# Kernel tuning notes

Measured on AMD Instinct MI355X. Metric: run time of the kernel, lower is better.

## Reference

```python
import jax, jax.numpy as jnp
import numpy as np

B, T, I, H = 32, 1024, 512, 512


def setup_inputs() -> dict:
    key = jax.random.key(0)
    ks = jax.random.split(key, 9)
    s = 0.05  # xavier-ish scale for 512-dim layers
    return {
        "x": jax.random.normal(ks[0], (B, T, I), jnp.float32),
        "W_in_0": jax.random.normal(ks[1], (I, H), jnp.float32) * s,
        "b_in_0": jnp.zeros((H,), jnp.float32),
        "W_h_0": jax.random.normal(ks[2], (H, 2 * H), jnp.float32) * s,
        "b_h_0": jnp.zeros((2 * H,), jnp.float32),
        "W_in_1": jax.random.normal(ks[3], (H, H), jnp.float32) * s,
        "b_in_1": jnp.zeros((H,), jnp.float32),
        "W_h_1": jax.random.normal(ks[4], (H, 2 * H), jnp.float32) * s,
        "b_h_1": jnp.zeros((2 * H,), jnp.float32),
    }


def _cell(ti, m_prev, c_prev, W_h, b_h, hid):
    # ti: transformed input [B,H]; gates from previous m (the "hidden")
    gates = m_prev @ W_h + b_h                 # [B,2H]
    retain = jax.nn.sigmoid(gates[:, :hid])
    merge = jax.nn.sigmoid(gates[:, hid:])
    c_next = jnp.tanh(c_prev + retain * ti)
    m_next = (1.0 - merge) * ti + merge * c_next
    return m_next, c_next


def reference(x, W_in_0, b_in_0, W_h_0, b_h_0, W_in_1, b_in_1, W_h_1, b_h_1):
    b, t, _ = x.shape
    hid = W_in_0.shape[1]
    # layer-0 input transform is independent of the recurrence: batch it over time
    ti0_all = jnp.swapaxes(x @ W_in_0 + b_in_0, 0, 1)  # [T,B,H]

    def step(carry, ti0):
        (m0, c0), (m1, c1) = carry
        m0n, c0n = _cell(ti0, m0, c0, W_h_0, b_h_0, hid)
        ti1 = m0n @ W_in_1 + b_in_1
        m1n, c1n = _cell(ti1, m1, c1, W_h_1, b_h_1, hid)
        out_t = jnp.stack([m0n, m1n], axis=1)  # [B,L,H]
        return ((m0n, c0n), (m1n, c1n)), out_t

    z = jnp.zeros((b, hid), x.dtype)
    init = ((z, z), (z, z))
    (h0, h1), outs = jax.lax.scan(step, init, ti0_all)
    output = jnp.swapaxes(outs, 0, 1)  # [B,T,L,H]
    final_c = jnp.stack([h0[1], h1[1]], axis=1)  # [B,L,H]
    con = jnp.broadcast_to(final_c[:, None], output.shape)  # [B,T,L,H]
    return (output, output, con)
```

## Files before the change

kernel.cpp:

```cpp
#include <hip/hip_runtime.h>


#define T_STEPS 1024

typedef __bf16 bf8 __attribute__((ext_vector_type(8)));
typedef float  f4  __attribute__((ext_vector_type(4)));
typedef unsigned u32x4 __attribute__((ext_vector_type(4)));

__device__ __forceinline__ f4 mfma16(bf8 a, bf8 b, f4 c) {
    return __builtin_amdgcn_mfma_f32_16x16x32_bf16(a, b, c, 0, 0, 0);
}
__device__ __forceinline__ float sigf(float x)     { return 1.f / (1.f + __expf(-x)); }
__device__ __forceinline__ float tanhfast(float x) { return 1.f - 2.f / (1.f + __expf(2.f * x)); }
__device__ __forceinline__ unsigned pack2(float lo, float hi) {
    union { __bf16 h; unsigned short u; } a, b;
    a.h = (__bf16)lo; b.h = (__bf16)hi;
    return ((unsigned)b.u << 16) | (unsigned)a.u;
}
__device__ __forceinline__ void wait_lds_ge(int* p, int tgt) {
    while (__hip_atomic_load(p, __ATOMIC_ACQUIRE, __HIP_MEMORY_SCOPE_WORKGROUP) < tgt)
        __builtin_amdgcn_s_sleep(1);
}
__device__ __forceinline__ void set_lds(int* p, int v) {
    __hip_atomic_store(p, v, __ATOMIC_RELEASE, __HIP_MEMORY_SCOPE_WORKGROUP);
}
__device__ __forceinline__ void poll_flags(const unsigned* fbase, unsigned tgt, int lane) {
    while (true) {
        unsigned v = 0xFFFFFFFFu;
        if (lane < 32)
            v = __hip_atomic_load(fbase + lane * 16, __ATOMIC_RELAXED,
                                  __HIP_MEMORY_SCOPE_AGENT);
        if (__ballot(v >= tgt) == ~0ull) break;
        __builtin_amdgcn_s_sleep(1);
    }
    __builtin_amdgcn_sched_barrier(0);
}


__global__ __launch_bounds__(256) void k_init(const float* __restrict__ x,
                                              const float* __restrict__ w_in0,
                                              __bf16* __restrict__ xbf,
                                              __bf16* __restrict__ w0hi,
                                              __bf16* __restrict__ w0lo,
                                              unsigned* __restrict__ ws)
{
    size_t id = (size_t)blockIdx.x * 256 + threadIdx.x;
    size_t gs = (size_t)gridDim.x * 256;
    for (size_t i = id; i < 34816; i += gs) ws[i] = 0u;
    for (size_t i = id; i < (size_t)16777216; i += gs) {
        size_t r = i >> 9, c = i & 511;
        size_t b = r & 31, t = r >> 5;
        xbf[i] = (__bf16)x[(((b << 10) + t) << 9) + c];
    }
    for (size_t i = id; i < (size_t)262144; i += gs) {
        size_t n = i >> 9, k = i & 511;
        float v = w_in0[(k << 9) + n];
        __bf16 h = (__bf16)v;
        w0hi[i] = h;
        w0lo[i] = (__bf16)(v - (float)h);
    }
}

__global__ __launch_bounds__(256) void k_pregemm(const __bf16* __restrict__ xbf,
                                                 const __bf16* __restrict__ w0hi,
                                                 const __bf16* __restrict__ w0lo,
                                                 const float* __restrict__ b_in0,
                                                 float* __restrict__ ti0)
{
    int tid = threadIdx.x, lane = tid & 63, wid = tid >> 6;
    int wg = blockIdx.x;
    int mbase = (wg & 511) * 64 + wid * 16;
    int nbase = (wg >> 9) * 128;
    int col = lane & 15, kgrp = lane >> 4;
    f4 acc[8];
#pragma unroll
    for (int i = 0; i < 8; ++i) acc[i] = (f4){0.f, 0.f, 0.f, 0.f};
    const __bf16* ap = xbf + (size_t)(mbase + col) * 512 + kgrp * 8;
    for (int kk = 0; kk < 16; ++kk) {
        bf8 a = *reinterpret_cast<const bf8*>(ap + kk * 32);
        const __bf16* wb = w0hi + (size_t)(nbase + col) * 512 + kk * 32 + kgrp * 8;
        const __bf16* wl = w0lo + (size_t)(nbase + col) * 512 + kk * 32 + kgrp * 8;
#pragma unroll
        for (int ct = 0; ct < 8; ++ct) {
            bf8 bh = *reinterpret_cast<const bf8*>(wb + (size_t)ct * 16 * 512);
            bf8 bl = *reinterpret_cast<const bf8*>(wl + (size_t)ct * 16 * 512);
            acc[ct] = mfma16(a, bh, acc[ct]);
            acc[ct] = mfma16(a, bl, acc[ct]);
        }
    }
#pragma unroll
    for (int ct = 0; ct < 8; ++ct) {
        int c = nbase + ct * 16 + col;
        float bias = b_in0[c];
#pragma unroll
        for (int r = 0; r < 4; ++r) {
            int row = mbase + kgrp * 4 + r;
            ti0[(size_t)row * 512 + c] = acc[ct][r] + bias;
        }
    }
}

__global__ __launch_bounds__(192, 1) void k_recur(
    const float* __restrict__ wh0, const float* __restrict__ bh0g,
    const float* __restrict__ win1, const float* __restrict__ bin1g,
    const float* __restrict__ wh1, const float* __restrict__ bh1g,
    const float* __restrict__ ti0,
    float* __restrict__ out,
    unsigned* __restrict__ ws)
{
    __shared__ __bf16 sW[9][8192];
    __shared__ float  sTi1[2][256];
    __shared__ float  sMn0[2][256];
    __shared__ float  sMn1[2][256];
    __shared__ float  sB[5][16];
    __shared__ int    sAready, sAout, sB1rdy, sBdone, sCdone;

    int tid = threadIdx.x, lane = tid & 63, wid = tid >> 6;
    int wg = blockIdx.x;
    int rank  = wg & 31;
    int mhalf = wg >> 5;

    unsigned* flagsA = ws + mhalf * 512;
    unsigned* flagsB = ws + 1024 + mhalf * 512;
    unsigned* ring0d = ws + 2048;
    unsigned* ring1d = ws + 18432;
    float* fc = (float*)(ws + 34816);

    int h0 = rank * 16;
    int col = lane & 15, kgrp = lane >> 4;
    int rbrow = mhalf * 16;

    for (int i = tid; i < 8192; i += 192) {
        int cl = i & 15, k = i >> 4;
        int sw = (cl * 512 + k) ^ ((cl & 7) << 3);
        float v0r = wh0[(size_t)k * 1024 + h0 + cl];
        float v0m = wh0[(size_t)k * 1024 + 512 + h0 + cl];
        float v1r = wh1[(size_t)k * 1024 + h0 + cl];
        float v1m = wh1[(size_t)k * 1024 + 512 + h0 + cl];
        float vt  = win1[(size_t)k * 512 + h0 + cl];
        __bf16 a;
        a = (__bf16)v0r; sW[0][sw] = a; sW[1][sw] = (__bf16)(v0r - (float)a);
        a = (__bf16)v0m; sW[2][sw] = a; sW[3][sw] = (__bf16)(v0m - (float)a);
        a = (__bf16)v1r; sW[4][sw] = a; sW[5][sw] = (__bf16)(v1r - (float)a);
        a = (__bf16)v1m; sW[6][sw] = a; sW[7][sw] = (__bf16)(v1m - (float)a);
        sW[8][sw] = (__bf16)vt;
    }
    if (tid < 16) {
        sB[0][tid] = bh0g[h0 + tid];
        sB[1][tid] = bh0g[512 + h0 + tid];
        sB[2][tid] = bh1g[h0 + tid];
        sB[3][tid] = bh1g[512 + h0 + tid];
        sB[4][tid] = bin1g[h0 + tid];
    }
    if (tid == 0) { sAready = -1; sAout = -1; sB1rdy = -1; sBdone = -1; sCdone = -1; }
    __syncthreads();

    float cs[4] = {0.f, 0.f, 0.f, 0.f};

    if (wid == 0) {
        float t0n[4];
#pragma unroll
        for (int r = 0; r < 4; ++r)
            asm volatile("global_load_dword %0, %1, off"
                         : "=v"(t0n[r])
                         : "v"(ti0 + ((size_t)(rbrow + kgrp * 4 + r)) * 512 + h0 + col));
        unsigned pv = 0;
#pragma unroll 1
        for (int ph = 0; ph <= T_STEPS; ++ph) {
            if (ph > 0) {
                asm volatile("s_waitcnt vmcnt(0)" ::: "memory");
                __builtin_amdgcn_sched_barrier(0);
                unsigned v = (lane < 32 && lane != rank) ? pv : 0xFFFFFFFFu;
                if (__ballot(v >= (unsigned)ph) != ~0ull)
                    poll_flags(flagsA, (unsigned)ph, lane);
                __builtin_amdgcn_sched_barrier(0);
            }
            u32x4 au[16];
            {
                const unsigned* rp = ring0d + ((ph + 1) & 1) * 8192
                                   + (rbrow + col) * 8 + (kgrp & 1) * 4;
#pragma unroll
                for (int kk = 0; kk < 16; ++kk)
                    asm volatile("global_load_dwordx4 %0, %1, off sc1"
                                 : "=v"(au[kk]) : "v"(rp + (2 * kk + (kgrp >> 1)) * 256));
            }
            f4 accR = {0.f, 0.f, 0.f, 0.f};
            f4 accM = {0.f, 0.f, 0.f, 0.f};
            f4 accT = {0.f, 0.f, 0.f, 0.f};
            asm volatile("s_waitcnt vmcnt(8)" ::: "memory");
            __builtin_amdgcn_sched_barrier(0);
#pragma unroll
            for (int kk = 0; kk < 8; ++kk) {
                union { u32x4 u; bf8 v; } A; A.u = au[kk];
                int e = (col * 512 + kk * 32 + kgrp * 8) ^ ((col & 7) << 3);
                accR = mfma16(A.v, *reinterpret_cast<const bf8*>(&sW[0][e]), accR);
                accR = mfma16(A.v, *reinterpret_cast<const bf8*>(&sW[1][e]), accR);
                accM = mfma16(A.v, *reinterpret_cast<const bf8*>(&sW[2][e]), accM);
                accM = mfma16(A.v, *reinterpret_cast<const bf8*>(&sW[3][e]), accM);
                accT = mfma16(A.v, *reinterpret_cast<const bf8*>(&sW[8][e]), accT);
            }
            asm volatile("s_waitcnt vmcnt(0)" ::: "memory");
            __builtin_amdgcn_sched_barrier(0);
#pragma unroll
            for (int kk = 8; kk < 16; ++kk) {
                union { u32x4 u; bf8 v; } A; A.u = au[kk];
                int e = (col * 512 + kk * 32 + kgrp * 8) ^ ((col & 7) << 3);
                accR = mfma16(A.v, *reinterpret_cast<const bf8*>(&sW[0][e]), accR);
                accR = mfma16(A.v, *reinterpret_cast<const bf8*>(&sW[1][e]), accR);
                accM = mfma16(A.v, *reinterpret_cast<const bf8*>(&sW[2][e]), accM);
                accM = mfma16(A.v, *reinterpret_cast<const bf8*>(&sW[3][e]), accM);
                accT = mfma16(A.v, *reinterpret_cast<const bf8*>(&sW[8][e]), accT);
            }

            float mn[4];
            if (ph < T_STEPS) {
#pragma unroll
                for (int r = 0; r < 4; ++r) {
                    float retain = sigf(accR[r] + sB[0][col]);
                    float merge  = sigf(accM[r] + sB[1][col]);
                    float cv = tanhfast(cs[r] + retain * t0n[r]);
                    cs[r] = cv;
                    mn[r] = (1.f - merge) * t0n[r] + merge * cv;
                }
#pragma unroll
                for (int r = 0; r < 4; ++r) {
                    float hi = __shfl_xor(mn[r], 1, 64);
                    if (!(col & 1)) {
                        int row = rbrow + kgrp * 4 + r;
                        __hip_atomic_store(&ring0d[(ph & 1) * 8192 + rank * 256 + row * 8 + (col >> 1)],
                                           pack2(mn[r], hi), __ATOMIC_RELAXED,
                                           __HIP_MEMORY_SCOPE_AGENT);
                    }
                }
                if (ph + 1 < T_STEPS) {
#pragma unroll
                    for (int r = 0; r < 4; ++r)
                        asm volatile("global_load_dword %0, %1, off"
                                     : "=v"(t0n[r])
                                     : "v"(ti0 + ((size_t)(ph + 1) * 32 + rbrow + kgrp * 4 + r) * 512 + h0 + col));
                }
                asm volatile("s_waitcnt vmcnt(0)" ::: "memory");
                if (lane == 0)
                    __hip_atomic_store(&flagsA[rank * 16], (unsigned)(ph + 1), __ATOMIC_RELAXED,
                                       __HIP_MEMORY_SCOPE_AGENT);
                if (lane < 32 && lane != rank)
                    asm volatile("global_load_dword %0, %1, off sc1"
                                 : "=v"(pv) : "v"(flagsA + lane * 16));
            }

            wait_lds_ge(&sBdone, ph - 2);
#pragma unroll
            for (int r = 0; r < 4; ++r)
                sTi1[ph & 1][(kgrp * 4 + r) * 16 + col] = accT[r] + sB[4][col];
            if (lane == 0) set_lds(&sAready, ph);

            if (ph < T_STEPS) {
                wait_lds_ge(&sCdone, ph - 2);
#pragma unroll
                for (int r = 0; r < 4; ++r)
                    sMn0[ph & 1][(kgrp * 4 + r) * 16 + col] = mn[r];
                if (lane == 0) set_lds(&sAout, ph);
            }
        }
#pragma unroll
        for (int r = 0; r < 4; ++r) {
            int b = rbrow + kgrp * 4 + r;
            fc[((size_t)b * 2 + 0) * 512 + h0 + col] = cs[r];
        }
    } else if (wid == 1) {
#pragma unroll 1
        for (int ph = 1; ph <= T_STEPS; ++ph) {
            if (ph >= 2) poll_flags(flagsB, (unsigned)(ph - 1), lane);
            u32x4 au[16];
            {
                const unsigned* rp = ring1d + (ph & 1) * 8192
                                   + (rbrow + col) * 8 + (kgrp & 1) * 4;
#pragma unroll
                for (int kk = 0; kk < 16; ++kk)
                    asm volatile("global_load_dwordx4 %0, %1, off sc1"
                                 : "=v"(au[kk]) : "v"(rp + (2 * kk + (kgrp >> 1)) * 256));
                asm volatile("s_waitcnt vmcnt(0)" ::: "memory");
                __builtin_amdgcn_sched_barrier(0);
            }
            f4 accR = {0.f, 0.f, 0.f, 0.f};
            f4 accM = {0.f, 0.f, 0.f, 0.f};
#pragma unroll
            for (int kk = 0; kk < 16; ++kk) {
                union { u32x4 u; bf8 v; } A; A.u = au[kk];
                int e = (col * 512 + kk * 32 + kgrp * 8) ^ ((col & 7) << 3);
                accR = mfma16(A.v, *reinterpret_cast<const bf8*>(&sW[4][e]), accR);
                accR = mfma16(A.v, *reinterpret_cast<const bf8*>(&sW[5][e]), accR);
                accM = mfma16(A.v, *reinterpret_cast<const bf8*>(&sW[6][e]), accM);
                accM = mfma16(A.v, *reinterpret_cast<const bf8*>(&sW[7][e]), accM);
            }
            wait_lds_ge(&sAready, ph);
            float t1v[4];
#pragma unroll
            for (int r = 0; r < 4; ++r)
                t1v[r] = sTi1[ph & 1][(kgrp * 4 + r) * 16 + col];
            if (lane == 0) set_lds(&sBdone, ph);
            float mn[4];
#pragma unroll
            for (int r = 0; r < 4; ++r) {
                float retain = sigf(accR[r] + sB[2][col]);
                float merge  = sigf(accM[r] + sB[3][col]);
                float cv = tanhfast(cs[r] + retain * t1v[r]);
                cs[r] = cv;
                mn[r] = (1.f - merge) * t1v[r] + merge * cv;
            }
#pragma unroll
            for (int r = 0; r < 4; ++r) {
                float hi = __shfl_xor(mn[r], 1, 64);
                if (!(col & 1)) {
                    int row = rbrow + kgrp * 4 + r;
                    __hip_atomic_store(&ring1d[((ph + 1) & 1) * 8192 + rank * 256 + row * 8 + (col >> 1)],
                                       pack2(mn[r], hi), __ATOMIC_RELAXED,
                                       __HIP_MEMORY_SCOPE_AGENT);
                }
            }
            asm volatile("s_waitcnt vmcnt(0)" ::: "memory");
            if (lane == 0)
                __hip_atomic_store(&flagsB[rank * 16], (unsigned)ph, __ATOMIC_RELAXED,
                                   __HIP_MEMORY_SCOPE_AGENT);
            wait_lds_ge(&sCdone, ph - 2);
#pragma unroll
            for (int r = 0; r < 4; ++r)
                sMn1[ph & 1][(kgrp * 4 + r) * 16 + col] = mn[r];
            if (lane == 0) set_lds(&sB1rdy, ph);
        }
#pragma unroll
        for (int r = 0; r < 4; ++r) {
            int b = rbrow + kgrp * 4 + r;
            fc[((size_t)b * 2 + 1) * 512 + h0 + col] = cs[r];
        }
    } else {
#pragma unroll 1
        for (int ph = 0; ph <= T_STEPS; ++ph) {
            float m0[4], m1[4];
            bool has0 = (ph < T_STEPS), has1 = (ph >= 1);
            if (has0) {
                wait_lds_ge(&sAout, ph);
#pragma unroll
                for (int r = 0; r < 4; ++r)
                    m0[r] = sMn0[ph & 1][(kgrp * 4 + r) * 16 + col];
            }
            if (has1) {
                wait_lds_ge(&sB1rdy, ph);
#pragma unroll
                for (int r = 0; r < 4; ++r)
                    m1[r] = sMn1[ph & 1][(kgrp * 4 + r) * 16 + col];
            }
            if (lane == 0) set_lds(&sCdone, ph);
            if (has0) {
#pragma unroll
                for (int r = 0; r < 4; ++r) {
                    int b = rbrow + kgrp * 4 + r;
                    size_t ob = ((size_t)b * 1024 + ph) * 1024 + h0 + col;
                    __builtin_nontemporal_store(m0[r], out + ob);
                    __builtin_nontemporal_store(m0[r], out + (size_t)33554432 + ob);
                }
            }
            if (has1) {
#pragma unroll
                for (int r = 0; r < 4; ++r) {
                    int b = rbrow + kgrp * 4 + r;
                    size_t ob = ((size_t)b * 1024 + (ph - 1)) * 1024 + 512 + h0 + col;
                    __builtin_nontemporal_store(m1[r], out + ob);
                    __builtin_nontemporal_store(m1[r], out + (size_t)33554432 + ob);
                }
            }
        }
    }
}

__global__ __launch_bounds__(256) void k_final(const float* __restrict__ fc,
                                               float* __restrict__ seg2)
{
    size_t id = (size_t)blockIdx.x * 256 + threadIdx.x;
    size_t gs = (size_t)gridDim.x * 256;
    for (size_t i = id; i < (size_t)8388608; i += gs) {
        size_t flat = i * 4;
        int h = (int)(flat & 511);
        int l = (int)((flat >> 9) & 1);
        int b = (int)(flat >> 20);
        f4 v = *reinterpret_cast<const f4*>(&fc[((size_t)b * 2 + l) * 512 + h]);
        *reinterpret_cast<f4*>(&seg2[flat]) = v;
    }
}

extern "C" void kernel_launch(void* const* d_in, const int* in_sizes, int n_in,
                              void* d_out, int out_size, void* d_ws, size_t ws_size,
                              hipStream_t stream)
{
    const float* x     = (const float*)d_in[0];
    const float* w_in0 = (const float*)d_in[1];
    const float* b_in0 = (const float*)d_in[2];
    const float* wh0   = (const float*)d_in[3];
    const float* bh0   = (const float*)d_in[4];
    const float* win1  = (const float*)d_in[5];
    const float* bin1  = (const float*)d_in[6];
    const float* wh1   = (const float*)d_in[7];
    const float* bh1   = (const float*)d_in[8];
    float* out = (float*)d_out;

    float*  seg2 = out + (size_t)2 * 33554432;
    float*  ti0  = seg2;
    __bf16* xbf  = (__bf16*)(ti0 + 16777216);
    __bf16* w0hi = xbf + 16777216;
    __bf16* w0lo = w0hi + 262144;

    k_init<<<1024, 256, 0, stream>>>(x, w_in0, xbf, w0hi, w0lo, (unsigned*)d_ws);
    k_pregemm<<<2048, 256, 0, stream>>>(xbf, w0hi, w0lo, b_in0, ti0);
    k_recur<<<64, 192, 0, stream>>>(wh0, bh0, win1, bin1, wh1, bh1, ti0, out,
                                    (unsigned*)d_ws);
    k_final<<<1024, 256, 0, stream>>>((const float*)((unsigned*)d_ws + 34816), seg2);
}
```

Measured before the change: 4.310 ms.

## Split layer-0 flag polling into halves to overlap ring loads with MFMA

Layer-0 polling of the 32 producer flags is split into two 16-flag halves. Once the upper half of K producers is ready, their ring data is loaded and its MFMAs are issued, and only then does the wave wait on the lower half. The earlier prefetched flag load (pv) is dropped and the ti0 loads become plain C loads instead of inline asm. This overlaps part of the matmul with waiting on slower producers, at the cost of two polling loops per step and losing the speculative flag prefetch.

```diff
diff --git a/kernel.cpp b/kernel.cpp
--- a/kernel.cpp
+++ b/kernel.cpp
@@ -30,6 +30,28 @@
         if (lane < 32)
             v = __hip_atomic_load(fbase + lane * 16, __ATOMIC_RELAXED,
                                   __HIP_MEMORY_SCOPE_AGENT);
+        if (__ballot(v >= tgt) == ~0ull) break;
+        __builtin_amdgcn_s_sleep(1);
+    }
+    __builtin_amdgcn_sched_barrier(0);
+}
+__device__ __forceinline__ void poll_h0(const unsigned* fbase, unsigned tgt, int lane) {
+    const unsigned* p = fbase + (lane & 15) * 16;
+    while (true) {
+        unsigned v = 0xFFFFFFFFu;
+        if (lane < 16)
+            v = __hip_atomic_load(p, __ATOMIC_RELAXED, __HIP_MEMORY_SCOPE_AGENT);
+        if (__ballot(v >= tgt) == ~0ull) break;
+        __builtin_amdgcn_s_sleep(1);
+    }
+    __builtin_amdgcn_sched_barrier(0);
+}
+__device__ __forceinline__ void poll_h2(const unsigned* fbase, unsigned tgt, int lane) {
+    const unsigned* p = fbase + (16 + (lane & 15)) * 16;
+    while (true) {
+        unsigned v = 0xFFFFFFFFu;
+        if (lane < 16)
+            v = __hip_atomic_load(p, __ATOMIC_RELAXED, __HIP_MEMORY_SCOPE_AGENT);
         if (__ballot(v >= tgt) == ~0ull) break;
         __builtin_amdgcn_s_sleep(1);
     }
@@ -161,55 +183,68 @@
         float t0n[4];
 #pragma unroll
         for (int r = 0; r < 4; ++r)
-            asm volatile("global_load_dword %0, %1, off"
-                         : "=v"(t0n[r])
-                         : "v"(ti0 + ((size_t)(rbrow + kgrp * 4 + r)) * 512 + h0 + col));
-        unsigned pv = 0;
+            t0n[r] = ti0[((size_t)(rbrow + kgrp * 4 + r)) * 512 + h0 + col];
 #pragma unroll 1
         for (int ph = 0; ph <= T_STEPS; ++ph) {
+            u32x4 au[16];
+            const unsigned* rp = ring0d + ((ph + 1) & 1) * 8192
+                               + (rbrow + col) * 8 + (kgrp & 1) * 4;
+            f4 accR = {0.f, 0.f, 0.f, 0.f};
+            f4 accM = {0.f, 0.f, 0.f, 0.f};
+            f4 accT = {0.f, 0.f, 0.f, 0.f};
+
             if (ph > 0) {
+                poll_h2(flagsA, (unsigned)ph, lane);
+#pragma unroll
+                for (int kk = 8; kk < 16; ++kk)
+                    asm volatile("global_load_dwordx4 %0, %1, off sc1"
+                                 : "=v"(au[kk]) : "v"(rp + (2 * kk + (kgrp >> 1)) * 256));
+                poll_h0(flagsA, (unsigned)ph, lane);
+#pragma unroll
+                for (int kk = 0; kk < 8; ++kk)
+                    asm volatile("global_load_dwordx4 %0, %1, off sc1"
+                                 : "=v"(au[kk]) : "v"(rp + (2 * kk + (kgrp >> 1)) * 256));
+                asm volatile("s_waitcnt vmcnt(8)" ::: "memory");
+                __builtin_amdgcn_sched_barrier(0);
+#pragma unroll
+                for (int kk = 8; kk < 16; ++kk) {
+                    union { u32x4 u; bf8 v; } A; A.u = au[kk];
+                    int e = (col * 512 + kk * 32 + kgrp * 8) ^ ((col & 7) << 3);
+                    accR = mfma16(A.v, *reinterpret_cast<const bf8*>(&sW[0][e]), accR);
+                    accR = mfma16(A.v, *reinterpret_cast<const bf8*>(&sW[1][e]), accR);
+                    accM = mfma16(A.v, *reinterpret_cast<const bf8*>(&sW[2][e]), accM);
+                    accM = mfma16(A.v, *reinterpret_cast<const bf8*>(&sW[3][e]), accM);
+                    accT = mfma16(A.v, *reinterpret_cast<const bf8*>(&sW[8][e]), accT);
+                }
                 asm volatile("s_waitcnt vmcnt(0)" ::: "memory");
                 __builtin_amdgcn_sched_barrier(0);
-                unsigned v = (lane < 32 && lane != rank) ? pv : 0xFFFFFFFFu;
-                if (__ballot(v >= (unsigned)ph) != ~0ull)
-                    poll_flags(flagsA, (unsigned)ph, lane);
-                __builtin_amdgcn_sched_barrier(0);
-            }
-            u32x4 au[16];
-            {
-                const unsigned* rp = ring0d + ((ph + 1) & 1) * 8192
-                                   + (rbrow + col) * 8 + (kgrp & 1) * 4;
+#pragma unroll
+                for (int kk = 0; kk < 8; ++kk) {
+                    union { u32x4 u; bf8 v; } A; A.u = au[kk];
+                    int e = (col * 512 + kk * 32 + kgrp * 8) ^ ((col & 7) << 3);
+                    accR = mfma16(A.v, *reinterpret_cast<const bf8*>(&sW[0][e]), accR);
+                    accR = mfma16(A.v, *reinterpret_cast<const bf8*>(&sW[1][e]), accR);
+                    accM = mfma16(A.v, *reinterpret_cast<const bf8*>(&sW[2][e]), accM);
+                    accM = mfma16(A.v, *reinterpret_cast<const bf8*>(&sW[3][e]), accM);
+                    accT = mfma16(A.v, *reinterpret_cast<const bf8*>(&sW[8][e]), accT);
+                }
+            } else {
 #pragma unroll
                 for (int kk = 0; kk < 16; ++kk)
                     asm volatile("global_load_dwordx4 %0, %1, off sc1"
                                  : "=v"(au[kk]) : "v"(rp + (2 * kk + (kgrp >> 1)) * 256));
-            }
-            f4 accR = {0.f, 0.f, 0.f, 0.f};
-            f4 accM = {0.f, 0.f, 0.f, 0.f};
-            f4 accT = {0.f, 0.f, 0.f, 0.f};
-            asm volatile("s_waitcnt vmcnt(8)" ::: "memory");
-            __builtin_amdgcn_sched_barrier(0);
-#pragma unroll
-            for (int kk = 0; kk < 8; ++kk) {
-                union { u32x4 u; bf8 v; } A; A.u = au[kk];
-                int e = (col * 512 + kk * 32 + kgrp * 8) ^ ((col & 7) << 3);
-                accR = mfma16(A.v, *reinterpret_cast<const bf8*>(&sW[0][e]), accR);
-                accR = mfma16(A.v, *reinterpret_cast<const bf8*>(&sW[1][e]), accR);
-                accM = mfma16(A.v, *reinterpret_cast<const bf8*>(&sW[2][e]), accM);
-                accM = mfma16(A.v, *reinterpret_cast<const bf8*>(&sW[3][e]), accM);
-                accT = mfma16(A.v, *reinterpret_cast<const bf8*>(&sW[8][e]), accT);
-            }
-            asm volatile("s_waitcnt vmcnt(0)" ::: "memory");
-            __builtin_amdgcn_sched_barrier(0);
-#pragma unroll
-            for (int kk = 8; kk < 16; ++kk) {
-                union { u32x4 u; bf8 v; } A; A.u = au[kk];
-                int e = (col * 512 + kk * 32 + kgrp * 8) ^ ((col & 7) << 3);
-                accR = mfma16(A.v, *reinterpret_cast<const bf8*>(&sW[0][e]), accR);
-                accR = mfma16(A.v, *reinterpret_cast<const bf8*>(&sW[1][e]), accR);
-                accM = mfma16(A.v, *reinterpret_cast<const bf8*>(&sW[2][e]), accM);
-                accM = mfma16(A.v, *reinterpret_cast<const bf8*>(&sW[3][e]), accM);
-                accT = mfma16(A.v, *reinterpret_cast<const bf8*>(&sW[8][e]), accT);
+                asm volatile("s_waitcnt vmcnt(0)" ::: "memory");
+                __builtin_amdgcn_sched_barrier(0);
+#pragma unroll
+                for (int kk = 0; kk < 16; ++kk) {
+                    union { u32x4 u; bf8 v; } A; A.u = au[kk];
+                    int e = (col * 512 + kk * 32 + kgrp * 8) ^ ((col & 7) << 3);
+                    accR = mfma16(A.v, *reinterpret_cast<const bf8*>(&sW[0][e]), accR);
+                    accR = mfma16(A.v, *reinterpret_cast<const bf8*>(&sW[1][e]), accR);
+                    accM = mfma16(A.v, *reinterpret_cast<const bf8*>(&sW[2][e]), accM);
+                    accM = mfma16(A.v, *reinterpret_cast<const bf8*>(&sW[3][e]), accM);
+                    accT = mfma16(A.v, *reinterpret_cast<const bf8*>(&sW[8][e]), accT);
+                }
             }
 
             float mn[4];
@@ -235,17 +270,12 @@
                 if (ph + 1 < T_STEPS) {
 #pragma unroll
                     for (int r = 0; r < 4; ++r)
-                        asm volatile("global_load_dword %0, %1, off"
-                                     : "=v"(t0n[r])
-                                     : "v"(ti0 + ((size_t)(ph + 1) * 32 + rbrow + kgrp * 4 + r) * 512 + h0 + col));
+                        t0n[r] = ti0[((size_t)(ph + 1) * 32 + rbrow + kgrp * 4 + r) * 512 + h0 + col];
                 }
                 asm volatile("s_waitcnt vmcnt(0)" ::: "memory");
                 if (lane == 0)
                     __hip_atomic_store(&flagsA[rank * 16], (unsigned)(ph + 1), __ATOMIC_RELAXED,
                                        __HIP_MEMORY_SCOPE_AGENT);
-                if (lane < 32 && lane != rank)
-                    asm volatile("global_load_dword %0, %1, off sc1"
-                                 : "=v"(pv) : "v"(flagsA + lane * 16));
             }
 
             wait_lds_ge(&sBdone, ph - 2);
```

New measurement: 4.660 ms. 8.1% more time.
